# Kernel tuning notes

Measured on AMD Instinct MI355X. Metric: run time of the kernel, lower is better.

Reference implementation:

```python
import jax, jax.numpy as jnp
import numpy as np

B, S, C, H, D = 4, 1024, 1024, 16, 64
MAX_POS = 512
SPAN = min(max(S, S), MAX_POS)  # rel_attn_span = 512
SCALE = 1.0 / np.sqrt(3.0 * D)


def setup_inputs() -> dict:
    key = jax.random.key(0)
    ks = jax.random.split(key, 10)
    std = 0.02
    return {
        "hidden_states": jax.random.normal(ks[0], (B, S, C), jnp.float32),
        "rel_embeddings": jax.random.normal(ks[1], (2 * MAX_POS, C), jnp.float32),
        "Wq": jax.random.normal(ks[2], (C, H, D), jnp.float32) * std,
        "bq": jnp.zeros((H, D), jnp.float32),
        "Wk": jax.random.normal(ks[3], (C, H, D), jnp.float32) * std,
        "Wv": jax.random.normal(ks[4], (C, H, D), jnp.float32) * std,
        "bv": jnp.zeros((H, D), jnp.float32),
        "Wc2p": jax.random.normal(ks[5], (C, H, D), jnp.float32) * std,
        "Wp2c": jax.random.normal(ks[6], (C, H, D), jnp.float32) * std,
        "bp2c": jnp.zeros((H, D), jnp.float32),
        "Wo": jax.random.normal(ks[7], (C, C), jnp.float32) * std,
        "bo": jnp.zeros((C,), jnp.float32),
    }


def reference(hidden_states, rel_embeddings, Wq, bq, Wk, Wv, bv, Wc2p, Wp2c, bp2c, Wo, bo):
    # Projections: 'abc,cde->abde'  -> [B,S,H,D]
    q = jnp.einsum("bsc,chd->bshd", hidden_states, Wq) + bq
    k = jnp.einsum("bsc,chd->bshd", hidden_states, Wk)
    v = jnp.einsum("bsc,chd->bshd", hidden_states, Wv) + bv

    q = q * SCALE
    # content-to-content scores: 'aecd,abcd->acbe' -> [B,H,Q,K]
    scores = jnp.einsum("bkhd,bqhd->bhqk", k, q)

    # relative-position ids: rel_pos[q,k] = q - k, shape [S,S]
    ids = jnp.arange(S, dtype=jnp.int32)
    rel_pos = ids[:, None] - ids[None, :]

    # slice rel table to the active span (full table here since S >= MAX_POS)
    rel = rel_embeddings[MAX_POS - SPAN : MAX_POS + SPAN, :]  # [2*SPAN, C]

    # c2p: pos_key [2*SPAN,H,D]; scores [B,H,Q,2*SPAN]; gather along last axis
    pos_key = jnp.einsum("rc,chd->rhd", rel, Wc2p)
    c2p = jnp.einsum("bqhd,rhd->bhqr", q, pos_key)
    c2p_pos = jnp.clip(rel_pos + SPAN, 0, 2 * SPAN - 1)  # [Q,K]
    c2p_idx = jnp.broadcast_to(c2p_pos[None, None], (B, H, S, S))
    c2p_g = jnp.take_along_axis(c2p, c2p_idx, axis=-1)

    # p2c: pos_query (scaled) [2*SPAN,H,D]; scores [B,H,K,2*SPAN]
    pos_query = (jnp.einsum("rc,chd->rhd", rel, Wp2c) + bp2c) * SCALE
    p2c = jnp.einsum("bkhd,rhd->bhkr", k, pos_query)
    p2c_pos = jnp.clip(-rel_pos + SPAN, 0, 2 * SPAN - 1)  # [K,K]
    p2c_idx = jnp.broadcast_to(p2c_pos[None, None], (B, H, S, S))
    p2c_g = jnp.take_along_axis(p2c, p2c_idx, axis=-1)

    scores = scores + c2p_g + p2c_g
    # NOTE: source calls _masked_softmax without passing attention_mask -> plain softmax
    probs = jax.nn.softmax(scores, axis=-1)

    # 'acbe,aecd->abcd' -> [B,Q,H,D]
    attn_out = jnp.einsum("bhqk,bkhd->bqhd", probs, v)
    attn_out = attn_out.reshape(B, S, H * D)
    return jnp.einsum("bsc,cd->bsd", attn_out, Wo) + bo
```

## Files before the change

kernel.cpp:

```cpp
#include <hip/hip_runtime.h>
#include <cmath>

#define SCALE_F 0.07216878364870322f

typedef unsigned short u16;
typedef __attribute__((ext_vector_type(8))) __bf16 bf16x8;
typedef __attribute__((ext_vector_type(4))) float f32x4;
typedef __attribute__((ext_vector_type(16))) float f32x16;

#define MFMA16(a, b, c) __builtin_amdgcn_mfma_f32_16x16x32_bf16(a, b, c, 0, 0, 0)
#define MFMA32(a, b, c) __builtin_amdgcn_mfma_f32_32x32x16_bf16(a, b, c, 0, 0, 0)

__device__ __forceinline__ u16 f2bf(float x) {
    unsigned u = __float_as_uint(x);
    unsigned r = (u + 0x7fffu + ((u >> 16) & 1u)) >> 16;
    return (u16)r;
}
__device__ __forceinline__ float bf2f(u16 u) {
    return __uint_as_float(((unsigned)u) << 16);
}
__device__ __forceinline__ void split2(float x, u16& h, u16& l) {
    h = f2bf(x);
    l = f2bf(x - bf2f(h));
}

__device__ __forceinline__ void glds16(const u16* g, u16* s) {
    __builtin_amdgcn_global_load_lds(
        (const __attribute__((address_space(1))) unsigned int*)g,
        (__attribute__((address_space(3))) unsigned int*)s,
        16, 0, 0);
}

__device__ __forceinline__ bf16x8 frg(const u16* base, int row, int ch) {
    return *(const bf16x8*)(base + (row << 6) + ((ch ^ (row & 7)) << 3));
}

__global__ __launch_bounds__(256) void split_rows2(
    const float* __restrict__ x0, u16* __restrict__ h0, u16* __restrict__ l0,
    int nblk0,
    const float* __restrict__ x1, u16* __restrict__ h1, u16* __restrict__ l1)
{
    const float* x; u16* h; u16* l; int bx = blockIdx.x;
    if (bx < nblk0) { x = x0; h = h0; l = l0; }
    else { x = x1; h = h1; l = l1; bx -= nblk0; }
    int i = (bx * 256 + threadIdx.x) << 2;
    float4 v = *(const float4*)(x + i);
    ushort4 hv, lv;
    split2(v.x, hv.x, lv.x); split2(v.y, hv.y, lv.y);
    split2(v.z, hv.z, lv.z); split2(v.w, hv.w, lv.w);
    *(ushort4*)(h + i) = hv;
    *(ushort4*)(l + i) = lv;
}

__global__ __launch_bounds__(256) void transpose3(
    const float* __restrict__ W0, u16* __restrict__ Th0, u16* __restrict__ Tl0,
    const float* __restrict__ W1, u16* __restrict__ Th1, u16* __restrict__ Tl1,
    const float* __restrict__ W2, u16* __restrict__ Th2, u16* __restrict__ Tl2)
{
    const float* W; u16* Th; u16* Tl;
    if (blockIdx.z == 0)      { W = W0; Th = Th0; Tl = Tl0; }
    else if (blockIdx.z == 1) { W = W1; Th = Th1; Tl = Tl1; }
    else                      { W = W2; Th = Th2; Tl = Tl2; }
    __shared__ float t[64][65];
    const int tid = threadIdx.x;
    const int r = tid >> 4, c4 = (tid & 15) << 2;
    const int k0 = blockIdx.y << 6, n0 = blockIdx.x << 6;
#pragma unroll
    for (int p = 0; p < 4; ++p) {
        int row = (p << 4) + r;
        float4 v = *(const float4*)(W + (size_t)(k0 + row) * 1024 + n0 + c4);
        t[row][c4] = v.x; t[row][c4 + 1] = v.y; t[row][c4 + 2] = v.z; t[row][c4 + 3] = v.w;
    }
    __syncthreads();
#pragma unroll
    for (int p = 0; p < 4; ++p) {
        int nr = (p << 4) + r;
        float a = t[c4 + 0][nr];
        float b = t[c4 + 1][nr];
        float c = t[c4 + 2][nr];
        float d = t[c4 + 3][nr];
        ushort4 hv, lv;
        split2(a, hv.x, lv.x); split2(b, hv.y, lv.y);
        split2(c, hv.z, lv.z); split2(d, hv.w, lv.w);
        *(ushort4*)(Th + (size_t)(n0 + nr) * 1024 + k0 + c4) = hv;
        *(ushort4*)(Tl + (size_t)(n0 + nr) * 1024 + k0 + c4) = lv;
    }
}

struct GD {
    const u16 *Ah, *Al, *Bh, *Bl;
    const float* bias;
    float* Cf;
    u16 *Ch, *Cl;
    int N, K;
    float scale;
    int mode;
};

__global__ __launch_bounds__(256, 2) void gemm_mfma(GD d0, GD d1, int xsplit)
{
    __shared__ u16 sAh[128 * 32];
    __shared__ u16 sAl[128 * 32];
    __shared__ u16 sBh[128 * 32];
    __shared__ u16 sBl[128 * 32];

    const GD d = (blockIdx.x < (unsigned)xsplit) ? d0 : d1;
    const int bx = (blockIdx.x < (unsigned)xsplit) ? blockIdx.x : blockIdx.x - xsplit;
    const int N = d.N, K = d.K;

    const int tid = threadIdx.x;
    const int wv = tid >> 6, lane = tid & 63;
    const int quad = lane >> 4, ln = lane & 15;
    const int wr = wv & 1, wc = wv >> 1;
    const int m0 = blockIdx.y << 7, n0 = bx << 7;

    const u16* gsrc = (wv == 0) ? d.Ah : (wv == 1) ? d.Al : (wv == 2) ? d.Bh : d.Bl;
    u16* sdst = (wv == 0) ? sAh : (wv == 1) ? sAl : (wv == 2) ? sBh : sBl;
    const int row0 = (wv < 2) ? m0 : n0;
    const u16* gbase = gsrc + (size_t)(row0 + (lane >> 2)) * K + ((lane & 3) << 3);

    f32x4 acc[4][4];
#pragma unroll
    for (int f = 0; f < 4; ++f)
#pragma unroll
        for (int g = 0; g < 4; ++g) acc[f][g] = (f32x4){0.f, 0.f, 0.f, 0.f};

    const u16* pa_h = sAh + ((wr << 6) + ln) * 32 + (quad << 3);
    const u16* pa_l = sAl + ((wr << 6) + ln) * 32 + (quad << 3);
    const u16* pb_h = sBh + ((wc << 6) + ln) * 32 + (quad << 3);
    const u16* pb_l = sBl + ((wc << 6) + ln) * 32 + (quad << 3);

    for (int kt = 0; kt < K; kt += 32) {
        __syncthreads();
#pragma unroll
        for (int t = 0; t < 8; ++t)
            glds16(gbase + (size_t)(t << 4) * K + kt, sdst + t * 512);
        __syncthreads();

        bf16x8 bhv[4], blv[4];
#pragma unroll
        for (int g = 0; g < 4; ++g) {
            bhv[g] = *(const bf16x8*)(pb_h + g * 512);
            blv[g] = *(const bf16x8*)(pb_l + g * 512);
        }
#pragma unroll
        for (int f = 0; f < 4; ++f) {
            bf16x8 xh = *(const bf16x8*)(pa_h + f * 512);
            bf16x8 xl = *(const bf16x8*)(pa_l + f * 512);
#pragma unroll
            for (int g = 0; g < 4; ++g) {
                acc[f][g] = MFMA16(xh, bhv[g], acc[f][g]);
                acc[f][g] = MFMA16(xh, blv[g], acc[f][g]);
                acc[f][g] = MFMA16(xl, bhv[g], acc[f][g]);
            }
        }
    }

    if (d.mode == 0) {
#pragma unroll
        for (int f = 0; f < 4; ++f) {
            int row = m0 + (wr << 6) + (f << 4) + (quad << 2);
#pragma unroll
            for (int g = 0; g < 4; ++g) {
                int col = n0 + (wc << 6) + (g << 4) + ln;
                float bb = d.bias ? d.bias[col] : 0.f;
#pragma unroll
                for (int r = 0; r < 4; ++r)
                    d.Cf[(size_t)(row + r) * N + col] = (acc[f][g][r] + bb) * d.scale;
            }
        }
    } else if (d.mode == 1) {
#pragma unroll
        for (int f = 0; f < 4; ++f) {
            int row = m0 + (wr << 6) + (f << 4) + (quad << 2);
#pragma unroll
            for (int g = 0; g < 4; ++g) {
                int col = n0 + (wc << 6) + (g << 4) + ln;
                float bb = d.bias ? d.bias[col] : 0.f;
#pragma unroll
                for (int r = 0; r < 4; ++r) {
                    float v = (acc[f][g][r] + bb) * d.scale;
                    u16 hh, ll;
                    split2(v, hh, ll);
                    d.Ch[(size_t)(row + r) * N + col] = hh;
                    d.Cl[(size_t)(row + r) * N + col] = ll;
                }
            }
        }
    } else if (d.mode == 2) {
#pragma unroll
        for (int f = 0; f < 4; ++f) {
            int row = m0 + (wr << 6) + (f << 4) + (quad << 2);
#pragma unroll
            for (int g = 0; g < 4; ++g) {
                int col = n0 + (wc << 6) + (g << 4) + ln;
                size_t obase = (size_t)(col >> 10) * 1048576 + (col & 1023);
#pragma unroll
                for (int r = 0; r < 4; ++r) {
                    float v = acc[f][g][r] + (d.bias ? d.bias[row + r] : 0.f);
                    u16 hh, ll;
                    split2(v, hh, ll);
                    size_t idx = obase + (size_t)(row + r) * 1024;
                    d.Ch[idx] = hh;
                    d.Cl[idx] = ll;
                }
            }
        }
    } else {
#pragma unroll
        for (int f = 0; f < 4; ++f) {
            int row = m0 + (wr << 6) + (f << 4) + (quad << 2);
#pragma unroll
            for (int g = 0; g < 4; ++g) {
                int col = n0 + (wc << 6) + (g << 4) + ln;
                float bb = d.bias ? d.bias[col] : 0.f;
#pragma unroll
                for (int r = 0; r < 4; ++r)
                    d.Ch[(size_t)(row + r) * N + col] =
                        f2bf((acc[f][g][r] + bb) * d.scale);
            }
        }
    }
}

__global__ __launch_bounds__(256, 2) void attn_mfma(
    const u16* Qh_g, const u16* Ql_g,
    const u16* __restrict__ Kh_g, const u16* __restrict__ Kl_g,
    const u16* __restrict__ VTh_g, const u16* __restrict__ VTl_g,
    const u16* __restrict__ PKh_g, const u16* __restrict__ PQh_g,
    u16* outh, u16* outl)
{
    __shared__ __align__(16) unsigned char smem[67840];
    u16* Kh_s  = (u16*)smem;
    u16* Kl_s  = (u16*)(smem + 8192);
    u16* PKs   = (u16*)(smem + 16384);
    u16* VTh_s = (u16*)(smem + 16384);
    u16* VTl_s = (u16*)(smem + 24576);
    u16* PQs   = (u16*)(smem + 32768);
    u16* Ph    = (u16*)(smem + 49152);
    u16* Pl    = (u16*)(smem + 58368);
    float* Mbase = (float*)(smem + 49152);
    float* l_s = (float*)(smem + 67584);

    const int tid = threadIdx.x;
    const int wv = tid >> 6, lane = tid & 63;
    const int half = lane >> 5, lc = lane & 31;
    const int rw = wv & 1, cw = wv >> 1;
    const int b = blockIdx.z, h = blockIdx.y;
    const int q0 = blockIdx.x << 6, hd0 = h << 6;
    float* Mw = Mbase + wv * 1056;

    const int rloc = lane >> 3;
    const int k4e  = (((lane & 7) ^ rloc) << 3);

    bf16x8 qfh[4], qfl[4], kfh[4], kfl[4];
    const size_t arow = ((size_t)(b * 1024 + q0 + (rw << 5) + lc) << 10) + hd0 + (half << 3);
    {
#pragma unroll
        for (int c = 0; c < 4; ++c) {
            qfh[c] = *(const bf16x8*)(Qh_g + arow + (c << 4));
            qfl[c] = *(const bf16x8*)(Ql_g + arow + (c << 4));
            kfh[c] = *(const bf16x8*)(Kh_g + arow + (c << 4));
            kfl[c] = *(const bf16x8*)(Kl_g + arow + (c << 4));
        }
    }
    if (tid < 64) l_s[tid] = 0.f;

    f32x16 o;
    float l_part[16];
#pragma unroll
    for (int r = 0; r < 16; ++r) { o[r] = 0.f; l_part[r] = 0.f; }

    const int sbC = (rw - cw + 1) << 5;
    const int sbP = (cw - rw + 1) << 5;

    {
#pragma unroll
        for (int t = 0; t < 2; ++t) {
            int call = wv + (t << 2);
            int row = (call << 3) + rloc;
            size_t g = ((size_t)(b * 1024 + 0 + row) << 10) + hd0 + k4e;
            glds16(Kh_g + g, Kh_s + (call << 9));
            glds16(Kl_g + g, Kl_s + (call << 9));
        }
        const int baseC = q0 + 449, baseP = -q0 + 449;
#pragma unroll
        for (int t = 0; t < 4; ++t) {
            int call = wv + (t << 2);
            int row = (call << 3) + rloc;
            int rc = min(max(baseC + row, 0), 1023);
            int rp = min(max(baseP + row, 0), 1023);
            glds16(PKh_g + (((size_t)rc << 10) + hd0 + k4e), PKs + (call << 9));
            glds16(PQh_g + (((size_t)rp << 10) + hd0 + k4e), PQs + (call << 9));
        }
    }
    __syncthreads();

    for (int kt = 0; kt < 16; ++kt) {
        const int k0 = kt << 6;
        f32x16 s;
#pragma unroll
        for (int r = 0; r < 16; ++r) s[r] = 0.f;
        {
            const int krow = (cw << 5) + lc;
#pragma unroll
            for (int c = 0; c < 4; ++c) {
                int ch = (c << 1) + half;
                bf16x8 bh = frg(Kh_s, krow, ch);
                bf16x8 bl = frg(Kl_s, krow, ch);
                s = MFMA32(qfh[c], bh, s);
                s = MFMA32(qfh[c], bl, s);
                s = MFMA32(qfl[c], bh, s);
            }
        }
        {
            f32x16 M0, M1;
#pragma unroll
            for (int r = 0; r < 16; ++r) { M0[r] = 0.f; M1[r] = 0.f; }
#pragma unroll
            for (int c = 0; c < 4; ++c) {
                int ch = (c << 1) + half;
                bf16x8 b0 = frg(PKs, sbC + lc, ch);
                bf16x8 b1 = frg(PKs, sbC + 32 + lc, ch);
                M0 = MFMA32(qfh[c], b0, M0); M0 = MFMA32(qfl[c], b0, M0);
                M1 = MFMA32(qfh[c], b1, M1); M1 = MFMA32(qfl[c], b1, M1);
            }
#pragma unroll
            for (int r = 0; r < 16; ++r) {
                int m = (r & 3) + ((r >> 2) << 3) + (half << 2);
                bool u = (lc >= m);
                float val = u ? M0[r] : M1[r];
                int nn = m - lc + (u ? 31 : -1);
                Mw[m * 33 + nn] = val;
            }
#pragma unroll
            for (int r = 0; r < 16; ++r) {
                int m = (r & 3) + ((r >> 2) << 3) + (half << 2);
                s[r] += Mw[m * 33 + lc];
            }
        }
        {
            f32x16 M0, M1;
#pragma unroll
            for (int r = 0; r < 16; ++r) { M0[r] = 0.f; M1[r] = 0.f; }
#pragma unroll
            for (int c = 0; c < 4; ++c) {
                int ch = (c << 1) + half;
                bf16x8 b0 = frg(PQs, sbP + lc, ch);
                bf16x8 b1 = frg(PQs, sbP + 32 + lc, ch);
                M0 = MFMA32(kfh[c], b0, M0); M0 = MFMA32(kfl[c], b0, M0);
                M1 = MFMA32(kfh[c], b1, M1); M1 = MFMA32(kfl[c], b1, M1);
            }
#pragma unroll
            for (int r = 0; r < 16; ++r) {
                int m = (r & 3) + ((r >> 2) << 3) + (half << 2);
                bool u = (lc >= 31 - m);
                float val = u ? M0[r] : M1[r];
                int nn = lc + m + (u ? -31 : 1);
                Mw[m * 33 + nn] = val;
            }
#pragma unroll
            for (int r = 0; r < 16; ++r) {
                int m = (r & 3) + ((r >> 2) << 3) + (half << 2);
                s[r] += Mw[m * 33 + lc];
            }
        }
#pragma unroll
        for (int r = 0; r < 16; ++r) {
            s[r] = __expf(s[r]);
            l_part[r] += s[r];
        }
        __syncthreads();
        {
#pragma unroll
            for (int t = 0; t < 2; ++t) {
                int call = wv + (t << 2);
                int row = (call << 3) + rloc;
                size_t g = ((size_t)((b * 16 + h) * 64 + row) << 10) + k0 + k4e;
                glds16(VTh_g + g, VTh_s + (call << 9));
                glds16(VTl_g + g, VTl_s + (call << 9));
            }
        }
#pragma unroll
        for (int r = 0; r < 16; ++r) {
            int m = (r & 3) + ((r >> 2) << 3) + (half << 2);
            int addr = ((rw << 5) + m) * 72 + (cw << 5) + lc;
            u16 hh, ll;
            split2(s[r], hh, ll);
            Ph[addr] = hh;
            Pl[addr] = ll;
        }
        __syncthreads();
        {
            const u16* ap  = Ph + ((rw << 5) + lc) * 72 + (half << 3);
            const u16* apl = Pl + ((rw << 5) + lc) * 72 + (half << 3);
            const int vrow = (cw << 5) + lc;
#pragma unroll
            for (int c = 0; c < 4; ++c) {
                int ch = (c << 1) + half;
                bf16x8 ah = *(const bf16x8*)(ap + (c << 4));
                bf16x8 al = *(const bf16x8*)(apl + (c << 4));
                bf16x8 bh = frg(VTh_s, vrow, ch);
                bf16x8 bl = frg(VTl_s, vrow, ch);
                o = MFMA32(ah, bh, o);
                o = MFMA32(ah, bl, o);
                o = MFMA32(al, bh, o);
            }
        }
        __syncthreads();
        {
            const int k0n = ((kt + 1) & 15) << 6;
#pragma unroll
            for (int t = 0; t < 2; ++t) {
                int call = wv + (t << 2);
                int row = (call << 3) + rloc;
                size_t g = ((size_t)(b * 1024 + k0n + row) << 10) + hd0 + k4e;
                glds16(Kh_g + g, Kh_s + (call << 9));
                glds16(Kl_g + g, Kl_s + (call << 9));
            }
            const int baseC = q0 - k0n + 449, baseP = k0n - q0 + 449;
#pragma unroll
            for (int t = 0; t < 4; ++t) {
                int call = wv + (t << 2);
                int row = (call << 3) + rloc;
                int rc = min(max(baseC + row, 0), 1023);
                int rp = min(max(baseP + row, 0), 1023);
                glds16(PKh_g + (((size_t)rc << 10) + hd0 + k4e), PKs + (call << 9));
                glds16(PQh_g + (((size_t)rp << 10) + hd0 + k4e), PQs + (call << 9));
            }
        }
        __syncthreads();
    }
#pragma unroll
    for (int r = 0; r < 16; ++r) {
        float v = l_part[r];
#pragma unroll
        for (int off = 1; off < 32; off <<= 1) v += __shfl_xor(v, off, 64);
        int m = (r & 3) + ((r >> 2) << 3) + (half << 2);
        if (lc == 0) atomicAdd(&l_s[(rw << 5) + m], v);
    }
    __syncthreads();
#pragma unroll
    for (int r = 0; r < 16; ++r) {
        int m = (r & 3) + ((r >> 2) << 3) + (half << 2);
        int row = (rw << 5) + m;
        float inv = 1.f / l_s[row];
        size_t g = ((size_t)(b * 1024 + q0 + row) << 10) + hd0 + (cw << 5) + lc;
        u16 hh, ll;
        split2(o[r] * inv, hh, ll);
        outh[g] = hh;
        outl[g] = ll;
    }
}

extern "C" void kernel_launch(void* const* d_in, const int* in_sizes, int n_in,
                              void* d_out, int out_size, void* d_ws, size_t ws_size,
                              hipStream_t stream)
{
    (void)in_sizes; (void)n_in; (void)out_size; (void)ws_size;
    const float* hidden = (const float*)d_in[0];
    const float* rel    = (const float*)d_in[1];
    const float* Wq   = (const float*)d_in[2];
    const float* bq   = (const float*)d_in[3];
    const float* Wk   = (const float*)d_in[4];
    const float* Wv   = (const float*)d_in[5];
    const float* bv   = (const float*)d_in[6];
    const float* Wc2p = (const float*)d_in[7];
    const float* Wp2c = (const float*)d_in[8];
    const float* bp2c = (const float*)d_in[9];
    const float* Wo   = (const float*)d_in[10];
    const float* bo   = (const float*)d_in[11];
    float* out = (float*)d_out;

    u16* U = (u16*)d_ws;
    const size_t MU = 1048576;
    u16* Hh  = U;              u16* Hl  = U + 4 * MU;
    u16* Rh  = U + 8 * MU;     u16* Rl  = U + 9 * MU;
    u16* WtAh = U + 10 * MU;   u16* WtAl = U + 11 * MU;
    u16* Qh  = U + 12 * MU;    u16* Ql  = U + 16 * MU;
    u16* Kh  = U + 20 * MU;    u16* Kl  = U + 24 * MU;
    u16* VTh = U + 28 * MU;    u16* VTl = U + 32 * MU;
    u16* WkTh = U + 28 * MU;   u16* WkTl = U + 29 * MU;
    u16* PKh = U + 0 * MU;
    u16* PQh = U + 2 * MU;
    u16* Wp2cTh = U + 4 * MU;  u16* Wp2cTl = U + 5 * MU;
    u16* WoTh = U + 6 * MU;    u16* WoTl = U + 7 * MU;

    dim3 blk(256);

    hipLaunchKernelGGL(split_rows2, dim3(5120), blk, 0, stream,
                       hidden, Hh, Hl, 4096, rel, Rh, Rl);

    hipLaunchKernelGGL(transpose3, dim3(16, 16, 2), blk, 0, stream,
                       Wq, WtAh, WtAl, Wk, WkTh, WkTl,
                       (const float*)nullptr, (u16*)nullptr, (u16*)nullptr);

    {
        GD dQ = {Hh, Hl, WtAh, WtAl, bq, nullptr, Qh, Ql, 1024, 1024, SCALE_F, 1};
        GD dK = {Hh, Hl, WkTh, WkTl, nullptr, nullptr, Kh, Kl, 1024, 1024, 1.f, 1};
        hipLaunchKernelGGL(gemm_mfma, dim3(16, 32), blk, 0, stream, dQ, dK, 8);
    }

    hipLaunchKernelGGL(transpose3, dim3(16, 16, 1), blk, 0, stream,
                       Wv, WtAh, WtAl,
                       (const float*)nullptr, (u16*)nullptr, (u16*)nullptr,
                       (const float*)nullptr, (u16*)nullptr, (u16*)nullptr);

    {
        GD dV = {WtAh, WtAl, Hh, Hl, bv, nullptr, VTh, VTl, 4096, 1024, 1.f, 2};
        hipLaunchKernelGGL(gemm_mfma, dim3(32, 8), blk, 0, stream, dV, dV, 9999);
    }

    hipLaunchKernelGGL(transpose3, dim3(16, 16, 3), blk, 0, stream,
                       Wc2p, WtAh, WtAl, Wp2c, Wp2cTh, Wp2cTl, Wo, WoTh, WoTl);

    {
        GD dPK = {Rh, Rl, WtAh, WtAl, nullptr, nullptr, PKh, nullptr, 1024, 1024, 1.f, 3};
        GD dPQ = {Rh, Rl, Wp2cTh, Wp2cTl, bp2c, nullptr, PQh, nullptr, 1024, 1024, SCALE_F, 3};
        hipLaunchKernelGGL(gemm_mfma, dim3(16, 8), blk, 0, stream, dPK, dPQ, 8);
    }

    hipLaunchKernelGGL(attn_mfma, dim3(16, 16, 4), blk, 0, stream,
                       Qh, Ql, Kh, Kl, VTh, VTl, PKh, PQh, Qh, Ql);

    {
        GD dO = {Qh, Ql, WoTh, WoTl, bo, out, nullptr, nullptr, 1024, 1024, 1.f, 0};
        hipLaunchKernelGGL(gemm_mfma, dim3(8, 32), blk, 0, stream, dO, dO, 9999);
    }
}
```

Baseline: 491.4 us.

## Restructure attention loop: shuffle-based rel-pos skew, prefetch V, fewer barriers

Replaces the LDS round-trip used to skew the c2p/p2c relative-position tiles with cross-lane shuffles, removing the per-wave scratch area. V tiles get their own LDS region and are prefetched together with K and position tiles for the next iteration, so the loop drops from four barriers to two. The P tile is now stored with an XOR swizzle instead of padded rows. MFMA accumulation chains are split into independent accumulators to shorten dependency chains. LDS use rises to 80KB, which may limit occupancy to fewer blocks per CU.

Result: slower. 666.9 us (+35.7%).

```diff
diff --git a/kernel.cpp b/kernel.cpp
--- a/kernel.cpp
+++ b/kernel.cpp
@@ -230,17 +230,16 @@
     const u16* __restrict__ PKh_g, const u16* __restrict__ PQh_g,
     u16* outh, u16* outl)
 {
-    __shared__ __align__(16) unsigned char smem[67840];
+    __shared__ __align__(16) unsigned char smem[81920];
     u16* Kh_s  = (u16*)smem;
     u16* Kl_s  = (u16*)(smem + 8192);
     u16* PKs   = (u16*)(smem + 16384);
-    u16* VTh_s = (u16*)(smem + 16384);
-    u16* VTl_s = (u16*)(smem + 24576);
     u16* PQs   = (u16*)(smem + 32768);
-    u16* Ph    = (u16*)(smem + 49152);
-    u16* Pl    = (u16*)(smem + 58368);
-    float* Mbase = (float*)(smem + 49152);
-    float* l_s = (float*)(smem + 67584);
+    u16* VTh_s = (u16*)(smem + 49152);
+    u16* VTl_s = (u16*)(smem + 57344);
+    u16* Ph    = (u16*)(smem + 65536);
+    u16* Pl    = (u16*)(smem + 73728);
+    float* l_s = (float*)(smem + 65536);
 
     const int tid = threadIdx.x;
     const int wv = tid >> 6, lane = tid & 63;
@@ -248,7 +247,8 @@
     const int rw = wv & 1, cw = wv >> 1;
     const int b = blockIdx.z, h = blockIdx.y;
     const int q0 = blockIdx.x << 6, hd0 = h << 6;
-    float* Mw = Mbase + wv * 1056;
+
+    const int h4 = half << 2, hsel = half << 5, lch = lc - h4;
 
     const int rloc = lane >> 3;
     const int k4e  = (((lane & 7) ^ rloc) << 3);
@@ -264,12 +264,11 @@
             kfl[c] = *(const bf16x8*)(Kl_g + arow + (c << 4));
         }
     }
-    if (tid < 64) l_s[tid] = 0.f;
-
-    f32x16 o;
+
+    f32x16 o0, o1;
     float l_part[16];
 #pragma unroll
-    for (int r = 0; r < 16; ++r) { o[r] = 0.f; l_part[r] = 0.f; }
+    for (int r = 0; r < 16; ++r) { o0[r] = 0.f; o1[r] = 0.f; l_part[r] = 0.f; }
 
     const int sbC = (rw - cw + 1) << 5;
     const int sbP = (cw - rw + 1) << 5;
@@ -279,9 +278,12 @@
         for (int t = 0; t < 2; ++t) {
             int call = wv + (t << 2);
             int row = (call << 3) + rloc;
-            size_t g = ((size_t)(b * 1024 + 0 + row) << 10) + hd0 + k4e;
+            size_t g = ((size_t)(b * 1024 + row) << 10) + hd0 + k4e;
             glds16(Kh_g + g, Kh_s + (call << 9));
             glds16(Kl_g + g, Kl_s + (call << 9));
+            size_t gv = ((size_t)((b * 16 + h) * 64 + row) << 10) + k4e;
+            glds16(VTh_g + gv, VTh_s + (call << 9));
+            glds16(VTl_g + gv, VTl_s + (call << 9));
         }
         const int baseC = q0 + 449, baseP = -q0 + 449;
 #pragma unroll
@@ -297,10 +299,9 @@
     __syncthreads();
 
     for (int kt = 0; kt < 16; ++kt) {
-        const int k0 = kt << 6;
-        f32x16 s;
-#pragma unroll
-        for (int r = 0; r < 16; ++r) s[r] = 0.f;
+        f32x16 s, sB;
+#pragma unroll
+        for (int r = 0; r < 16; ++r) { s[r] = 0.f; sB[r] = 0.f; }
         {
             const int krow = (cw << 5) + lc;
 #pragma unroll
@@ -308,11 +309,14 @@
                 int ch = (c << 1) + half;
                 bf16x8 bh = frg(Kh_s, krow, ch);
                 bf16x8 bl = frg(Kl_s, krow, ch);
-                s = MFMA32(qfh[c], bh, s);
-                s = MFMA32(qfh[c], bl, s);
-                s = MFMA32(qfl[c], bh, s);
-            }
-        }
+                s  = MFMA32(qfh[c], bh, s);
+                sB = MFMA32(qfh[c], bl, sB);
+                s  = MFMA32(qfl[c], bh, s);
+            }
+        }
+#pragma unroll
+        for (int r = 0; r < 16; ++r) s[r] += sB[r];
+
         {
             f32x16 M0, M1;
 #pragma unroll
@@ -322,21 +326,19 @@
                 int ch = (c << 1) + half;
                 bf16x8 b0 = frg(PKs, sbC + lc, ch);
                 bf16x8 b1 = frg(PKs, sbC + 32 + lc, ch);
-                M0 = MFMA32(qfh[c], b0, M0); M0 = MFMA32(qfl[c], b0, M0);
-                M1 = MFMA32(qfh[c], b1, M1); M1 = MFMA32(qfl[c], b1, M1);
-            }
+                M0 = MFMA32(qfh[c], b0, M0);
+                M1 = MFMA32(qfh[c], b1, M1);
+                M0 = MFMA32(qfl[c], b0, M0);
+                M1 = MFMA32(qfl[c], b1, M1);
+            }
+            const int dd = h4 - 1 - lc;
 #pragma unroll
             for (int r = 0; r < 16; ++r) {
-                int m = (r & 3) + ((r >> 2) << 3) + (half << 2);
-                bool u = (lc >= m);
-                float val = u ? M0[r] : M1[r];
-                int nn = m - lc + (u ? 31 : -1);
-                Mw[m * 33 + nn] = val;
-            }
-#pragma unroll
-            for (int r = 0; r < 16; ++r) {
-                int m = (r & 3) + ((r >> 2) << 3) + (half << 2);
-                s[r] += Mw[m * 33 + lc];
+                const int m_lo = (r & 3) + ((r >> 2) << 3);
+                int src = ((m_lo + dd) & 31) | hsel;
+                float a0 = __shfl(M0[r], src, 64);
+                float a1 = __shfl(M1[r], src, 64);
+                s[r] += (lch >= m_lo) ? a0 : a1;
             }
         }
         {
@@ -348,68 +350,50 @@
                 int ch = (c << 1) + half;
                 bf16x8 b0 = frg(PQs, sbP + lc, ch);
                 bf16x8 b1 = frg(PQs, sbP + 32 + lc, ch);
-                M0 = MFMA32(kfh[c], b0, M0); M0 = MFMA32(kfl[c], b0, M0);
-                M1 = MFMA32(kfh[c], b1, M1); M1 = MFMA32(kfl[c], b1, M1);
-            }
+                M0 = MFMA32(kfh[c], b0, M0);
+                M1 = MFMA32(kfh[c], b1, M1);
+                M0 = MFMA32(kfl[c], b0, M0);
+                M1 = MFMA32(kfl[c], b1, M1);
+            }
+            const int de = lc - h4 - 1;
 #pragma unroll
             for (int r = 0; r < 16; ++r) {
-                int m = (r & 3) + ((r >> 2) << 3) + (half << 2);
-                bool u = (lc >= 31 - m);
-                float val = u ? M0[r] : M1[r];
-                int nn = lc + m + (u ? -31 : 1);
-                Mw[m * 33 + nn] = val;
-            }
+                const int m_lo = (r & 3) + ((r >> 2) << 3);
+                int src = ((de - m_lo) & 31) | hsel;
+                float a0 = __shfl(M0[r], src, 64);
+                float a1 = __shfl(M1[r], src, 64);
+                s[r] += (lch <= m_lo) ? a0 : a1;
+            }
+        }
+        {
+            const int cx3 = ((((cw << 2) + (lc >> 3)) ^ h4) << 3);
+            const int cole = lc & 7;
+            const int rb = (rw << 5) + h4;
 #pragma unroll
             for (int r = 0; r < 16; ++r) {
-                int m = (r & 3) + ((r >> 2) << 3) + (half << 2);
-                s[r] += Mw[m * 33 + lc];
-            }
-        }
-#pragma unroll
-        for (int r = 0; r < 16; ++r) {
-            s[r] = __expf(s[r]);
-            l_part[r] += s[r];
-        }
-        __syncthreads();
+                const int m_lo = (r & 3) + ((r >> 2) << 3);
+                float ev = __expf(s[r]);
+                l_part[r] += ev;
+                u16 hh, ll;
+                split2(ev, hh, ll);
+                int addr = ((rb + m_lo) << 6) + ((cx3 ^ ((r & 3) << 3)) | cole);
+                Ph[addr] = hh;
+                Pl[addr] = ll;
+            }
+        }
+        bf16x8 vth[4], vtl[4];
         {
-#pragma unroll
-            for (int t = 0; t < 2; ++t) {
-                int call = wv + (t << 2);
-                int row = (call << 3) + rloc;
-                size_t g = ((size_t)((b * 16 + h) * 64 + row) << 10) + k0 + k4e;
-                glds16(VTh_g + g, VTh_s + (call << 9));
-                glds16(VTl_g + g, VTl_s + (call << 9));
-            }
-        }
-#pragma unroll
-        for (int r = 0; r < 16; ++r) {
-            int m = (r & 3) + ((r >> 2) << 3) + (half << 2);
-            int addr = ((rw << 5) + m) * 72 + (cw << 5) + lc;
-            u16 hh, ll;
-            split2(s[r], hh, ll);
-            Ph[addr] = hh;
-            Pl[addr] = ll;
-        }
-        __syncthreads();
-        {
-            const u16* ap  = Ph + ((rw << 5) + lc) * 72 + (half << 3);
-            const u16* apl = Pl + ((rw << 5) + lc) * 72 + (half << 3);
             const int vrow = (cw << 5) + lc;
 #pragma unroll
             for (int c = 0; c < 4; ++c) {
                 int ch = (c << 1) + half;
-                bf16x8 ah = *(const bf16x8*)(ap + (c << 4));
-                bf16x8 al = *(const bf16x8*)(apl + (c << 4));
-                bf16x8 bh = frg(VTh_s, vrow, ch);
-                bf16x8 bl = frg(VTl_s, vrow, ch);
-                o = MFMA32(ah, bh, o);
-                o = MFMA32(ah, bl, o);
-                o = MFMA32(al, bh, o);
+                vth[c] = frg(VTh_s, vrow, ch);
+                vtl[c] = frg(VTl_s, vrow, ch);
             }
         }
         __syncthreads();
-        {
-            const int k0n = ((kt + 1) & 15) << 6;
+        if (kt < 15) {
+            const int k0n = (kt + 1) << 6;
 #pragma unroll
             for (int t = 0; t < 2; ++t) {
                 int call = wv + (t << 2);
@@ -417,6 +401,9 @@
                 size_t g = ((size_t)(b * 1024 + k0n + row) << 10) + hd0 + k4e;
                 glds16(Kh_g + g, Kh_s + (call << 9));
                 glds16(Kl_g + g, Kl_s + (call << 9));
+                size_t gv = ((size_t)((b * 16 + h) * 64 + row) << 10) + k0n + k4e;
+                glds16(VTh_g + gv, VTh_s + (call << 9));
+                glds16(VTl_g + gv, VTl_s + (call << 9));
             }
             const int baseC = q0 - k0n + 449, baseP = k0n - q0 + 449;
 #pragma unroll
@@ -429,25 +416,42 @@
                 glds16(PQh_g + (((size_t)rp << 10) + hd0 + k4e), PQs + (call << 9));
             }
         }
+        {
+            const int prow = (rw << 5) + lc;
+#pragma unroll
+            for (int c = 0; c < 4; ++c) {
+                int ch = (c << 1) + half;
+                bf16x8 ah = frg(Ph, prow, ch);
+                bf16x8 al = frg(Pl, prow, ch);
+                o0 = MFMA32(ah, vth[c], o0);
+                o1 = MFMA32(ah, vtl[c], o1);
+                o0 = MFMA32(al, vth[c], o0);
+            }
+        }
         __syncthreads();
     }
+
+    if (tid < 64) l_s[tid] = 0.f;
+    __syncthreads();
 #pragma unroll
     for (int r = 0; r < 16; ++r) {
         float v = l_part[r];
 #pragma unroll
         for (int off = 1; off < 32; off <<= 1) v += __shfl_xor(v, off, 64);
-        int m = (r & 3) + ((r >> 2) << 3) + (half << 2);
-        if (lc == 0) atomicAdd(&l_s[(rw << 5) + m], v);
+        if (lc == 0) {
+            const int m_lo = (r & 3) + ((r >> 2) << 3);
+            atomicAdd(&l_s[(rw << 5) + m_lo + h4], v);
+        }
     }
     __syncthreads();
 #pragma unroll
     for (int r = 0; r < 16; ++r) {
-        int m = (r & 3) + ((r >> 2) << 3) + (half << 2);
-        int row = (rw << 5) + m;
+        const int m_lo = (r & 3) + ((r >> 2) << 3);
+        int row = (rw << 5) + m_lo + h4;
         float inv = 1.f / l_s[row];
         size_t g = ((size_t)(b * 1024 + q0 + row) << 10) + hd0 + (cw << 5) + lc;
         u16 hh, ll;
-        split2(o[r] * inv, hh, ll);
+        split2((o0[r] + o1[r]) * inv, hh, ll);
         outh[g] = hh;
         outl[g] = ll;
     }
```

## Give V tiles their own LDS buffer and overlap loads with score compute

Applied to the files above, without the earlier changes.

The V^T tile now has a dedicated LDS region instead of aliasing the positional-key buffer. The next V tile is prefetched after the PV MFMA, and the next K/PK/PQ tiles are issued right after score computation, so loads overlap other work instead of sitting between barriers. The P matrix moves to a 64-wide XOR-swizzled layout read through the same fragment helper, and the M scratch buffers drop their padding. LDS per block grows to 80 KB, which may cut occupancy below the two blocks per CU the launch bounds request, and the unpadded M stride may cause bank conflicts.

After: 756.2 us. 53.9% more time.

```diff
diff --git a/kernel.cpp b/kernel.cpp
--- a/kernel.cpp
+++ b/kernel.cpp
@@ -230,17 +230,17 @@
     const u16* __restrict__ PKh_g, const u16* __restrict__ PQh_g,
     u16* outh, u16* outl)
 {
-    __shared__ __align__(16) unsigned char smem[67840];
+    __shared__ __align__(16) unsigned char smem[81920];
     u16* Kh_s  = (u16*)smem;
     u16* Kl_s  = (u16*)(smem + 8192);
     u16* PKs   = (u16*)(smem + 16384);
-    u16* VTh_s = (u16*)(smem + 16384);
-    u16* VTl_s = (u16*)(smem + 24576);
     u16* PQs   = (u16*)(smem + 32768);
-    u16* Ph    = (u16*)(smem + 49152);
-    u16* Pl    = (u16*)(smem + 58368);
-    float* Mbase = (float*)(smem + 49152);
-    float* l_s = (float*)(smem + 67584);
+    u16* VTh_s = (u16*)(smem + 49152);
+    u16* VTl_s = (u16*)(smem + 57344);
+    u16* Ph    = (u16*)(smem + 65536);
+    u16* Pl    = (u16*)(smem + 73728);
+    float* Mbase = (float*)(smem + 65536);
+    float* l_s = (float*)smem;
 
     const int tid = threadIdx.x;
     const int wv = tid >> 6, lane = tid & 63;
@@ -248,7 +248,8 @@
     const int rw = wv & 1, cw = wv >> 1;
     const int b = blockIdx.z, h = blockIdx.y;
     const int q0 = blockIdx.x << 6, hd0 = h << 6;
-    float* Mw = Mbase + wv * 1056;
+    float* Mw = Mbase + (wv << 10);
+    const int h4 = half << 2;
 
     const int rloc = lane >> 3;
     const int k4e  = (((lane & 7) ^ rloc) << 3);
@@ -264,7 +265,6 @@
             kfl[c] = *(const bf16x8*)(Kl_g + arow + (c << 4));
         }
     }
-    if (tid < 64) l_s[tid] = 0.f;
 
     f32x16 o;
     float l_part[16];
@@ -279,9 +279,12 @@
         for (int t = 0; t < 2; ++t) {
             int call = wv + (t << 2);
             int row = (call << 3) + rloc;
-            size_t g = ((size_t)(b * 1024 + 0 + row) << 10) + hd0 + k4e;
+            size_t g = ((size_t)(b * 1024 + row) << 10) + hd0 + k4e;
             glds16(Kh_g + g, Kh_s + (call << 9));
             glds16(Kl_g + g, Kl_s + (call << 9));
+            size_t gv = ((size_t)((b * 16 + h) * 64 + row) << 10) + k4e;
+            glds16(VTh_g + gv, VTh_s + (call << 9));
+            glds16(VTl_g + gv, VTl_s + (call << 9));
         }
         const int baseC = q0 + 449, baseP = -q0 + 449;
 #pragma unroll
@@ -297,7 +300,6 @@
     __syncthreads();
 
     for (int kt = 0; kt < 16; ++kt) {
-        const int k0 = kt << 6;
         f32x16 s;
 #pragma unroll
         for (int r = 0; r < 16; ++r) s[r] = 0.f;
@@ -327,16 +329,16 @@
             }
 #pragma unroll
             for (int r = 0; r < 16; ++r) {
-                int m = (r & 3) + ((r >> 2) << 3) + (half << 2);
+                int m = (r & 3) + ((r >> 2) << 3) + h4;
                 bool u = (lc >= m);
                 float val = u ? M0[r] : M1[r];
                 int nn = m - lc + (u ? 31 : -1);
-                Mw[m * 33 + nn] = val;
+                Mw[(m << 5) + nn] = val;
             }
 #pragma unroll
             for (int r = 0; r < 16; ++r) {
-                int m = (r & 3) + ((r >> 2) << 3) + (half << 2);
-                s[r] += Mw[m * 33 + lc];
+                int m = (r & 3) + ((r >> 2) << 3) + h4;
+                s[r] += Mw[(m << 5) + lc];
             }
         }
         {
@@ -353,63 +355,21 @@
             }
 #pragma unroll
             for (int r = 0; r < 16; ++r) {
-                int m = (r & 3) + ((r >> 2) << 3) + (half << 2);
+                int m = (r & 3) + ((r >> 2) << 3) + h4;
                 bool u = (lc >= 31 - m);
                 float val = u ? M0[r] : M1[r];
                 int nn = lc + m + (u ? -31 : 1);
-                Mw[m * 33 + nn] = val;
+                Mw[(m << 5) + nn] = val;
             }
 #pragma unroll
             for (int r = 0; r < 16; ++r) {
-                int m = (r & 3) + ((r >> 2) << 3) + (half << 2);
-                s[r] += Mw[m * 33 + lc];
-            }
-        }
-#pragma unroll
-        for (int r = 0; r < 16; ++r) {
-            s[r] = __expf(s[r]);
-            l_part[r] += s[r];
+                int m = (r & 3) + ((r >> 2) << 3) + h4;
+                s[r] += Mw[(m << 5) + lc];
+            }
         }
         __syncthreads();
-        {
-#pragma unroll
-            for (int t = 0; t < 2; ++t) {
-                int call = wv + (t << 2);
-                int row = (call << 3) + rloc;
-                size_t g = ((size_t)((b * 16 + h) * 64 + row) << 10) + k0 + k4e;
-                glds16(VTh_g + g, VTh_s + (call << 9));
-                glds16(VTl_g + g, VTl_s + (call << 9));
-            }
-        }
-#pragma unroll
-        for (int r = 0; r < 16; ++r) {
-            int m = (r & 3) + ((r >> 2) << 3) + (half << 2);
-            int addr = ((rw << 5) + m) * 72 + (cw << 5) + lc;
-            u16 hh, ll;
-            split2(s[r], hh, ll);
-            Ph[addr] = hh;
-            Pl[addr] = ll;
-        }
-        __syncthreads();
-        {
-            const u16* ap  = Ph + ((rw << 5) + lc) * 72 + (half << 3);
-            const u16* apl = Pl + ((rw << 5) + lc) * 72 + (half << 3);
-            const int vrow = (cw << 5) + lc;
-#pragma unroll
-            for (int c = 0; c < 4; ++c) {
-                int ch = (c << 1) + half;
-                bf16x8 ah = *(const bf16x8*)(ap + (c << 4));
-                bf16x8 al = *(const bf16x8*)(apl + (c << 4));
-                bf16x8 bh = frg(VTh_s, vrow, ch);
-                bf16x8 bl = frg(VTl_s, vrow, ch);
-                o = MFMA32(ah, bh, o);
-                o = MFMA32(ah, bl, o);
-                o = MFMA32(al, bh, o);
-            }
-        }
-        __syncthreads();
-        {
-            const int k0n = ((kt + 1) & 15) << 6;
+        if (kt < 15) {
+            const int k0n = (kt + 1) << 6;
 #pragma unroll
             for (int t = 0; t < 2; ++t) {
                 int call = wv + (t << 2);
@@ -429,20 +389,69 @@
                 glds16(PQh_g + (((size_t)rp << 10) + hd0 + k4e), PQs + (call << 9));
             }
         }
+        {
+            const int cx3 = ((((cw << 2) + (lc >> 3)) ^ h4) << 3);
+            const int cole = lc & 7;
+            const int rb = (rw << 5) + h4;
+#pragma unroll
+            for (int r = 0; r < 16; ++r) {
+                const int m_lo = (r & 3) + ((r >> 2) << 3);
+                float ev = __expf(s[r]);
+                l_part[r] += ev;
+                u16 hh, ll;
+                split2(ev, hh, ll);
+                int addr = ((rb + m_lo) << 6) + ((cx3 ^ ((r & 3) << 3)) | cole);
+                Ph[addr] = hh;
+                Pl[addr] = ll;
+            }
+        }
         __syncthreads();
-    }
+        {
+            const int prow = (rw << 5) + lc;
+            const int vrow = (cw << 5) + lc;
+#pragma unroll
+            for (int c = 0; c < 4; ++c) {
+                int ch = (c << 1) + half;
+                bf16x8 ah = frg(Ph, prow, ch);
+                bf16x8 al = frg(Pl, prow, ch);
+                bf16x8 bh = frg(VTh_s, vrow, ch);
+                bf16x8 bl = frg(VTl_s, vrow, ch);
+                o = MFMA32(ah, bh, o);
+                o = MFMA32(ah, bl, o);
+                o = MFMA32(al, bh, o);
+            }
+        }
+        __syncthreads();
+        if (kt < 15) {
+            const int k0n = (kt + 1) << 6;
+#pragma unroll
+            for (int t = 0; t < 2; ++t) {
+                int call = wv + (t << 2);
+                int row = (call << 3) + rloc;
+                size_t gv = ((size_t)((b * 16 + h) * 64 + row) << 10) + k0n + k4e;
+                glds16(VTh_g + gv, VTh_s + (call << 9));
+                glds16(VTl_g + gv, VTl_s + (call << 9));
+            }
+        }
+        __syncthreads();
+    }
+
+    if (tid < 64) l_s[tid] = 0.f;
+    __syncthreads();
 #pragma unroll
     for (int r = 0; r < 16; ++r) {
         float v = l_part[r];
 #pragma unroll
         for (int off = 1; off < 32; off <<= 1) v += __shfl_xor(v, off, 64);
-        int m = (r & 3) + ((r >> 2) << 3) + (half << 2);
-        if (lc == 0) atomicAdd(&l_s[(rw << 5) + m], v);
+        if (lc == 0) {
+            int m = (r & 3) + ((r >> 2) << 3) + h4;
+            atomicAdd(&l_s[(rw << 5) + m], v);
+        }
     }
     __syncthreads();
 #pragma unroll
     for (int r = 0; r < 16; ++r) {
-        int m = (r & 3) + ((r >> 2) << 3) + (half << 2);
+        int m = (r & 3) + ((r >> 2) << 3) + h4;
         int row = (rw << 5) + m;
         float inv = 1.f / l_s[row];
         size_t g = ((size_t)(b * 1024 + q0 + row) << 10) + hd0 + (cw << 5) + lc;
```
